# Kernel optimization log

Hardware: AMD Instinct MI355X
Metric: run time of the kernel (lower is better)

## Reference

```python
import jax, jax.numpy as jnp
import numpy as np

N = 100000   # num nodes (in_channels)
D = 128      # out_channels
H = 2 * D    # hidden dim
E = 1600000  # num edges


def gcn_conv(x, W, b, src, dst, dinv):
    """PyG GCNConv: linear -> symmetric-normalized aggregation (with self loops) -> +bias."""
    xw = x @ W                                   # [N, out]
    norm = dinv[src] * dinv[dst]                 # [E]
    msg = xw[src] * norm[:, None]                # [E, out]  gather + scale
    agg = jax.ops.segment_sum(msg, dst, num_segments=N)  # scatter-add to targets
    agg = agg + xw * (dinv * dinv)[:, None]      # self-loop contribution
    return agg + b


def setup_inputs() -> dict:
    key = jax.random.key(0)
    k1, k2, k3, k4, k5, k6 = jax.random.split(key, 6)
    emb = jax.random.normal(k1, (N, D), dtype=jnp.float32)
    # Glorot-ish scaled weights
    W1 = jax.random.normal(k2, (D, H), dtype=jnp.float32) * (1.0 / np.sqrt(D))
    b1 = jnp.zeros((H,), dtype=jnp.float32)
    W2 = jax.random.normal(k3, (H, D), dtype=jnp.float32) * (1.0 / np.sqrt(H))
    b2 = jnp.zeros((D,), dtype=jnp.float32)
    edge_index = jax.random.randint(k4, (2, E), 0, N, dtype=jnp.int32).astype(jnp.int64)
    return {"emb": emb, "W1": W1, "b1": b1, "W2": W2, "b2": b2, "edge_index": edge_index}


def reference(emb, W1, b1, W2, b2, edge_index):
    src = edge_index[0]
    dst = edge_index[1]
    # degrees include the self loop added by GCNConv (add_self_loops=True)
    deg = jax.ops.segment_sum(jnp.ones((E,), dtype=emb.dtype), dst, num_segments=N) + 1.0
    dinv = jax.lax.rsqrt(deg)                    # deg >= 1, always finite
    x = gcn_conv(emb, W1, b1, src, dst, dinv)    # [N, 2D]
    x = jax.nn.relu(x)
    out = gcn_conv(x, W2, b2, src, dst, dinv)    # [N, D]
    return out
```

## Files before the change

kernel.cpp:

```cpp
#include <hip/hip_runtime.h>
#include <hip/hip_bf16.h>

#define NN 100000
#define DD 128
#define HH 256

#define NBKT 391
#define ABLK 128

typedef _Float16 half_t;
typedef _Float16 half8 __attribute__((ext_vector_type(8)));
typedef _Float16 half4_t __attribute__((ext_vector_type(4)));
typedef float floatx4 __attribute__((ext_vector_type(4)));


__global__ __launch_bounds__(256) void hist_bkt(const int* __restrict__ dst,
                                                int* __restrict__ cnt,
                                                int* __restrict__ tot,
                                                int E, int epb) {
    __shared__ int h[NBKT];
    for (int i = threadIdx.x; i < NBKT; i += 256) h[i] = 0;
    __syncthreads();
    int base = blockIdx.x * epb;
    int end = min(base + epb, E);
    for (int e = base + (int)threadIdx.x; e < end; e += 256)
        atomicAdd(&h[dst[e] >> 8], 1);
    __syncthreads();
    for (int i = threadIdx.x; i < NBKT; i += 256) {
        int v = h[i];
        cnt[i * ABLK + blockIdx.x] = v;
        if (v) atomicAdd(&tot[i], v);
    }
}

__global__ __launch_bounds__(512) void scan_bkt(const int* __restrict__ tot,
                                                int* __restrict__ bktStart, int E) {
    __shared__ int s[512];
    int t = threadIdx.x;
    int v = (t < NBKT) ? tot[t] : 0;
    s[t] = v;
    __syncthreads();
    for (int off = 1; off < 512; off <<= 1) {
        int u = (t >= off) ? s[t - off] : 0;
        __syncthreads();
        s[t] += u;
        __syncthreads();
    }
    if (t < NBKT) bktStart[t] = s[t] - v;
    if (t == 0) bktStart[NBKT] = E;
}

__global__ __launch_bounds__(128) void scan_blkoff(const int* __restrict__ cnt,
                                                   const int* __restrict__ bktStart,
                                                   int* __restrict__ blockOff) {
    __shared__ int s[128];
    int b = blockIdx.x, t = threadIdx.x;
    int v = cnt[b * ABLK + t];
    s[t] = v;
    __syncthreads();
    for (int off = 1; off < 128; off <<= 1) {
        int u = (t >= off) ? s[t - off] : 0;
        __syncthreads();
        s[t] += u;
        __syncthreads();
    }
    blockOff[b * ABLK + t] = bktStart[b] + s[t] - v;
}

__global__ __launch_bounds__(256) void part_edges(const int* __restrict__ src,
                                                  const int* __restrict__ dst,
                                                  const int* __restrict__ blockOff,
                                                  int* __restrict__ psrc,
                                                  int* __restrict__ pdst,
                                                  int E, int epb) {
    __shared__ int lbase[NBKT];
    for (int i = threadIdx.x; i < NBKT; i += 256)
        lbase[i] = blockOff[i * ABLK + blockIdx.x];
    __syncthreads();
    int base = blockIdx.x * epb;
    int end = min(base + epb, E);
    for (int e = base + (int)threadIdx.x; e < end; e += 256) {
        int d = dst[e];
        int p = atomicAdd(&lbase[d >> 8], 1);
        psrc[p] = src[e];
        pdst[p] = d;
    }
}

__global__ __launch_bounds__(256) void build_csr(const int* __restrict__ psrc,
                                                 const int* __restrict__ pdst,
                                                 const int* __restrict__ bktStart,
                                                 int* __restrict__ offsets,
                                                 float* __restrict__ dinv,
                                                 int* __restrict__ eidx, int N) {
    __shared__ int ncnt[256];
    __shared__ int noff[256];
    __shared__ int cur[256];
    int b = blockIdx.x, t = threadIdx.x;
    int n0 = b << 8;
    int estart = bktStart[b], eend = bktStart[b + 1];
    ncnt[t] = 0;
    __syncthreads();
    for (int e = estart + t; e < eend; e += 256)
        atomicAdd(&ncnt[pdst[e] - n0], 1);
    __syncthreads();
    int c = ncnt[t];
    noff[t] = c;
    __syncthreads();
    for (int off = 1; off < 256; off <<= 1) {
        int u = (t >= off) ? noff[t - off] : 0;
        __syncthreads();
        noff[t] += u;
        __syncthreads();
    }
    int myoff = estart + noff[t] - c;
    cur[t] = myoff;
    int node = n0 + t;
    if (node < N) {
        offsets[node] = myoff;
        dinv[node] = rsqrtf((float)c + 1.0f);
        if (node == N - 1) offsets[N] = eend;
    }
    __syncthreads();
    for (int e = estart + t; e < eend; e += 256) {
        int d = pdst[e];
        int p = atomicAdd(&cur[d - n0], 1);
        eidx[p] = psrc[e];
    }
}

__global__ __launch_bounds__(256) void f2h_scale(const float* __restrict__ in,
                                                 const float* __restrict__ dinv,
                                                 half_t* __restrict__ out, int n4) {
    int i = blockIdx.x * 256 + threadIdx.x;
    if (i < n4) {
        float s = dinv[i >> 5];
        float4 v = ((const float4*)in)[i];
        half4_t o = {(half_t)(v.x * s), (half_t)(v.y * s), (half_t)(v.z * s), (half_t)(v.w * s)};
        ((half4_t*)out)[i] = o;
    }
}

__global__ __launch_bounds__(256) void transpose_w(const float* __restrict__ W,
                                                   half_t* __restrict__ Wt, int K, int C) {
    int i = blockIdx.x * 256 + threadIdx.x;
    if (i < K * C) {
        int k = i / C, c = i - k * C;
        Wt[(size_t)c * K + k] = (half_t)W[i];
    }
}

template <int K, int CT, bool BIASRELU>
__global__ __launch_bounds__(256) void gemm_mfma(const half_t* __restrict__ A,
                                                 const half_t* __restrict__ Bt,
                                                 const float* __restrict__ dinv,
                                                 const float* __restrict__ bias,
                                                 half_t* __restrict__ C, int M) {
    constexpr int BK = 64;
    constexpr int LDA = 72;
    __shared__ __align__(16) half_t As[128][LDA];
    __shared__ __align__(16) half_t Bs[64][LDA];

    const int tid = threadIdx.x;
    const int wave = tid >> 6, lane = tid & 63;
    const int wr = wave >> 1, wc = wave & 1;
    const int row0 = blockIdx.y * 128;
    const int col0 = blockIdx.x * 64;
    const int lrow = lane & 15, kq = lane >> 4;

    floatx4 acc[4][2] = {};

    for (int k0 = 0; k0 < K; k0 += BK) {
#pragma unroll
        for (int i = 0; i < 4; ++i) {
            int r = (tid >> 3) + i * 32;
            int kk = (tid & 7) * 8;
            int gr = row0 + r;
            half8 v = {};
            if (gr < M) v = *(const half8*)(A + (size_t)gr * K + k0 + kk);
            *(half8*)&As[r][kk] = v;
        }
#pragma unroll
        for (int i = 0; i < 2; ++i) {
            int n = (tid >> 3) + i * 32;
            int kk = (tid & 7) * 8;
            half8 v = *(const half8*)(Bt + (size_t)(col0 + n) * K + k0 + kk);
            *(half8*)&Bs[n][kk] = v;
        }
        __syncthreads();
#pragma unroll
        for (int ks = 0; ks < 2; ++ks) {
            half8 af[4], bf[2];
#pragma unroll
            for (int i = 0; i < 4; ++i)
                af[i] = *(const half8*)&As[wr * 64 + i * 16 + lrow][ks * 32 + kq * 8];
#pragma unroll
            for (int j = 0; j < 2; ++j)
                bf[j] = *(const half8*)&Bs[wc * 32 + j * 16 + lrow][ks * 32 + kq * 8];
#pragma unroll
            for (int i = 0; i < 4; ++i)
#pragma unroll
                for (int j = 0; j < 2; ++j)
                    acc[i][j] = __builtin_amdgcn_mfma_f32_16x16x32_f16(af[i], bf[j], acc[i][j], 0, 0, 0);
        }
        __syncthreads();
    }

#pragma unroll
    for (int i = 0; i < 4; ++i) {
#pragma unroll
        for (int r = 0; r < 4; ++r) {
            int grow = row0 + wr * 64 + i * 16 + kq * 4 + r;
            if (grow < M) {
                float s = BIASRELU ? 0.f : dinv[grow];
#pragma unroll
                for (int j = 0; j < 2; ++j) {
                    int gcol = col0 + wc * 32 + j * 16 + lrow;
                    float v = acc[i][j][r];
                    if (BIASRELU) v = fmaxf(v + bias[gcol], 0.f);
                    else          v = v * s;
                    C[(size_t)grow * CT + gcol] = (half_t)v;
                }
            }
        }
    }
}

template <bool OUT16>
__global__ __launch_bounds__(256) void gather128(const half_t* __restrict__ y,
                                                 void* __restrict__ outv,
                                                 const int* __restrict__ offsets,
                                                 const int* __restrict__ eidx,
                                                 const float* __restrict__ dinv,
                                                 const float* __restrict__ bias, int N) {
    int node = blockIdx.x * 8 + (threadIdx.x >> 5);
    if (node >= N) return;
    int c = (threadIdx.x & 31) * 4;

    half4_t sv = *(const half4_t*)(y + (size_t)node * DD + c);
    float a0 = (float)sv[0], a1 = (float)sv[1], a2 = (float)sv[2], a3 = (float)sv[3];
    float b0 = 0.f, b1_ = 0.f, b2_ = 0.f, b3 = 0.f;

    int e = offsets[node];
    const int e1 = offsets[node + 1];
    for (; e + 3 < e1; e += 4) {
        int s0 = eidx[e], s1 = eidx[e + 1], s2 = eidx[e + 2], s3 = eidx[e + 3];
        half4_t v0 = *(const half4_t*)(y + (size_t)s0 * DD + c);
        half4_t v1 = *(const half4_t*)(y + (size_t)s1 * DD + c);
        half4_t v2 = *(const half4_t*)(y + (size_t)s2 * DD + c);
        half4_t v3 = *(const half4_t*)(y + (size_t)s3 * DD + c);
        a0 += (float)v0[0]; a1 += (float)v0[1]; a2 += (float)v0[2]; a3 += (float)v0[3];
        b0 += (float)v1[0]; b1_ += (float)v1[1]; b2_ += (float)v1[2]; b3 += (float)v1[3];
        a0 += (float)v2[0]; a1 += (float)v2[1]; a2 += (float)v2[2]; a3 += (float)v2[3];
        b0 += (float)v3[0]; b1_ += (float)v3[1]; b2_ += (float)v3[2]; b3 += (float)v3[3];
    }
    for (; e < e1; ++e) {
        int s0 = eidx[e];
        half4_t v0 = *(const half4_t*)(y + (size_t)s0 * DD + c);
        a0 += (float)v0[0]; a1 += (float)v0[1]; a2 += (float)v0[2]; a3 += (float)v0[3];
    }

    float s = dinv[node];
    float o0 = s * (a0 + b0);
    float o1 = s * (a1 + b1_);
    float o2 = s * (a2 + b2_);
    float o3 = s * (a3 + b3);
    if (OUT16) {
        half4_t o = {(half_t)o0, (half_t)o1, (half_t)o2, (half_t)o3};
        *(half4_t*)((half_t*)outv + (size_t)node * DD + c) = o;
    } else {
        float4 bb = *(const float4*)(bias + c);
        float4 o = make_float4(o0 + bb.x, o1 + bb.y, o2 + bb.z, o3 + bb.w);
        *(float4*)((float*)outv + (size_t)node * DD + c) = o;
    }
}

extern "C" void kernel_launch(void* const* d_in, const int* in_sizes, int n_in,
                              void* d_out, int out_size, void* d_ws, size_t ws_size,
                              hipStream_t stream) {
    const float* emb = (const float*)d_in[0];
    const float* W1  = (const float*)d_in[1];
    const float* b1  = (const float*)d_in[2];
    const float* W2  = (const float*)d_in[3];
    const float* b2  = (const float*)d_in[4];
    const int*   ei  = (const int*)d_in[5];

    const int N = NN;
    const int E = in_sizes[5] / 2;
    const int* src = ei;
    const int* dst = ei + E;

    char* w = (char*)d_ws;
    float*  dinv = (float*)w;  w += 100032 * 4;
    half_t* zh   = (half_t*)w; w += (size_t)NN * DD * 2;
    half_t* g1h  = (half_t*)w; w += (size_t)NN * DD * 2;
    half_t* x1h  = (half_t*)w; w += (size_t)NN * HH * 2;
    half_t* W1t  = (half_t*)w; w += (size_t)DD * HH * 2;
    half_t* W2t  = (half_t*)w; w += (size_t)HH * DD * 2;
    int* offsets = (int*)w;    w += 100032 * 4;
    int* cnt     = (int*)w;    w += (size_t)NBKT * ABLK * 4;
    int* blockOff= (int*)w;    w += (size_t)NBKT * ABLK * 4;
    int* tot     = (int*)w;    w += 512 * 4;
    int* bktStart= (int*)w;    w += 512 * 4;
    int* psrc    = (int*)w;    w += (size_t)E * 4;
    int* pdst    = (int*)w;    w += (size_t)E * 4;
    int* eidx    = (int*)w;
    float* out   = (float*)d_out;
    half_t* y2h  = zh;

    const int epb = (E + ABLK - 1) / ABLK;

    hipMemsetAsync(tot, 0, NBKT * sizeof(int), stream);
    hist_bkt<<<ABLK, 256, 0, stream>>>(dst, cnt, tot, E, epb);
    scan_bkt<<<1, 512, 0, stream>>>(tot, bktStart, E);
    scan_blkoff<<<NBKT, 128, 0, stream>>>(cnt, bktStart, blockOff);
    part_edges<<<ABLK, 256, 0, stream>>>(src, dst, blockOff, psrc, pdst, E, epb);
    build_csr<<<NBKT, 256, 0, stream>>>(psrc, pdst, bktStart, offsets, dinv, eidx, N);

    f2h_scale<<<(NN * DD / 4 + 255) / 256, 256, 0, stream>>>(emb, dinv, zh, NN * DD / 4);
    transpose_w<<<(DD * HH + 255) / 256, 256, 0, stream>>>(W1, W1t, DD, HH);
    transpose_w<<<(HH * DD + 255) / 256, 256, 0, stream>>>(W2, W2t, HH, DD);

    const int gy = (N + 127) / 128;
    const int aggBlocks = (N + 7) / 8;

    gather128<true><<<aggBlocks, 256, 0, stream>>>(zh, g1h, offsets, eidx, dinv, nullptr, N);
    gemm_mfma<DD, HH, true><<<dim3(HH / 64, gy), 256, 0, stream>>>(g1h, W1t, dinv, b1, x1h, N);

    gemm_mfma<HH, DD, false><<<dim3(DD / 64, gy), 256, 0, stream>>>(x1h, W2t, dinv, nullptr, y2h, N);
    gather128<false><<<aggBlocks, 256, 0, stream>>>(y2h, (void*)out, offsets, eidx, dinv, b2, N);
}
```

Before: 403.7 us.

## Pack partitioned edges into one word and slice gather across column blocks

Edge partitioning now stores the source index and the low 8 bits of the destination in a single int, so only one array is written and read between partition and CSR build. The gather kernel changes from 32 lanes per node over all 128 columns to 8 lanes per node over a 32-column slice. Four block groups cover the four slices, which shrinks the per-pass row footprint and may improve cache locality for the random source rows. The cost is that each edge index list is read four times, and each gathered row segment is 64 bytes instead of 256. Packing requires source indices below 2^23, which holds for N=100000.

```diff
diff --git a/kernel.cpp b/kernel.cpp
--- a/kernel.cpp
+++ b/kernel.cpp
@@ -70,8 +70,7 @@
 __global__ __launch_bounds__(256) void part_edges(const int* __restrict__ src,
                                                   const int* __restrict__ dst,
                                                   const int* __restrict__ blockOff,
-                                                  int* __restrict__ psrc,
-                                                  int* __restrict__ pdst,
+                                                  int* __restrict__ pedge,
                                                   int E, int epb) {
     __shared__ int lbase[NBKT];
     for (int i = threadIdx.x; i < NBKT; i += 256)
@@ -82,13 +81,11 @@
     for (int e = base + (int)threadIdx.x; e < end; e += 256) {
         int d = dst[e];
         int p = atomicAdd(&lbase[d >> 8], 1);
-        psrc[p] = src[e];
-        pdst[p] = d;
-    }
-}
-
-__global__ __launch_bounds__(256) void build_csr(const int* __restrict__ psrc,
-                                                 const int* __restrict__ pdst,
+        pedge[p] = (src[e] << 8) | (d & 255);
+    }
+}
+
+__global__ __launch_bounds__(256) void build_csr(const int* __restrict__ pedge,
                                                  const int* __restrict__ bktStart,
                                                  int* __restrict__ offsets,
                                                  float* __restrict__ dinv,
@@ -97,12 +94,11 @@
     __shared__ int noff[256];
     __shared__ int cur[256];
     int b = blockIdx.x, t = threadIdx.x;
-    int n0 = b << 8;
     int estart = bktStart[b], eend = bktStart[b + 1];
     ncnt[t] = 0;
     __syncthreads();
     for (int e = estart + t; e < eend; e += 256)
-        atomicAdd(&ncnt[pdst[e] - n0], 1);
+        atomicAdd(&ncnt[pedge[e] & 255], 1);
     __syncthreads();
     int c = ncnt[t];
     noff[t] = c;
@@ -115,7 +111,7 @@
     }
     int myoff = estart + noff[t] - c;
     cur[t] = myoff;
-    int node = n0 + t;
+    int node = (b << 8) + t;
     if (node < N) {
         offsets[node] = myoff;
         dinv[node] = rsqrtf((float)c + 1.0f);
@@ -123,9 +119,9 @@
     }
     __syncthreads();
     for (int e = estart + t; e < eend; e += 256) {
-        int d = pdst[e];
-        int p = atomicAdd(&cur[d - n0], 1);
-        eidx[p] = psrc[e];
+        int v = pedge[e];
+        int p = atomicAdd(&cur[v & 255], 1);
+        eidx[p] = v >> 8;
     }
 }
 
@@ -227,15 +223,16 @@
 }
 
 template <bool OUT16>
-__global__ __launch_bounds__(256) void gather128(const half_t* __restrict__ y,
-                                                 void* __restrict__ outv,
-                                                 const int* __restrict__ offsets,
-                                                 const int* __restrict__ eidx,
-                                                 const float* __restrict__ dinv,
-                                                 const float* __restrict__ bias, int N) {
-    int node = blockIdx.x * 8 + (threadIdx.x >> 5);
+__global__ __launch_bounds__(256) void gather_slice(const half_t* __restrict__ y,
+                                                    void* __restrict__ outv,
+                                                    const int* __restrict__ offsets,
+                                                    const int* __restrict__ eidx,
+                                                    const float* __restrict__ dinv,
+                                                    const float* __restrict__ bias, int N) {
+    int slice = blockIdx.x & 3;
+    int node = (blockIdx.x >> 2) * 32 + (threadIdx.x >> 3);
     if (node >= N) return;
-    int c = (threadIdx.x & 31) * 4;
+    int c = slice * 32 + (threadIdx.x & 7) * 4;
 
     half4_t sv = *(const half4_t*)(y + (size_t)node * DD + c);
     float a0 = (float)sv[0], a1 = (float)sv[1], a2 = (float)sv[2], a3 = (float)sv[3];
@@ -302,8 +299,7 @@
     int* blockOff= (int*)w;    w += (size_t)NBKT * ABLK * 4;
     int* tot     = (int*)w;    w += 512 * 4;
     int* bktStart= (int*)w;    w += 512 * 4;
-    int* psrc    = (int*)w;    w += (size_t)E * 4;
-    int* pdst    = (int*)w;    w += (size_t)E * 4;
+    int* pedge   = (int*)w;    w += (size_t)E * 4;
     int* eidx    = (int*)w;
     float* out   = (float*)d_out;
     half_t* y2h  = zh;
@@ -314,19 +310,19 @@
     hist_bkt<<<ABLK, 256, 0, stream>>>(dst, cnt, tot, E, epb);
     scan_bkt<<<1, 512, 0, stream>>>(tot, bktStart, E);
     scan_blkoff<<<NBKT, 128, 0, stream>>>(cnt, bktStart, blockOff);
-    part_edges<<<ABLK, 256, 0, stream>>>(src, dst, blockOff, psrc, pdst, E, epb);
-    build_csr<<<NBKT, 256, 0, stream>>>(psrc, pdst, bktStart, offsets, dinv, eidx, N);
+    part_edges<<<ABLK, 256, 0, stream>>>(src, dst, blockOff, pedge, E, epb);
+    build_csr<<<NBKT, 256, 0, stream>>>(pedge, bktStart, offsets, dinv, eidx, N);
 
     f2h_scale<<<(NN * DD / 4 + 255) / 256, 256, 0, stream>>>(emb, dinv, zh, NN * DD / 4);
     transpose_w<<<(DD * HH + 255) / 256, 256, 0, stream>>>(W1, W1t, DD, HH);
     transpose_w<<<(HH * DD + 255) / 256, 256, 0, stream>>>(W2, W2t, HH, DD);
 
     const int gy = (N + 127) / 128;
-    const int aggBlocks = (N + 7) / 8;
-
-    gather128<true><<<aggBlocks, 256, 0, stream>>>(zh, g1h, offsets, eidx, dinv, nullptr, N);
+    const int aggBlocks = 4 * ((N + 31) / 32);
+
+    gather_slice<true><<<aggBlocks, 256, 0, stream>>>(zh, g1h, offsets, eidx, dinv, nullptr, N);
     gemm_mfma<DD, HH, true><<<dim3(HH / 64, gy), 256, 0, stream>>>(g1h, W1t, dinv, b1, x1h, N);
 
     gemm_mfma<HH, DD, false><<<dim3(DD / 64, gy), 256, 0, stream>>>(x1h, W2t, dinv, nullptr, y2h, N);
-    gather128<false><<<aggBlocks, 256, 0, stream>>>(y2h, (void*)out, offsets, eidx, dinv, b2, N);
-}
+    gather_slice<false><<<aggBlocks, 256, 0, stream>>>(y2h, (void*)out, offsets, eidx, dinv, b2, N);
+}
```

Result: slower. 475.4 us (+17.8%).
